# Optimization experiments

Hardware: AMD Instinct MI355X
Metric: run time of the kernel (lower is better)

The kernel has to match this reference:

```python
import jax, jax.numpy as jnp
import numpy as np

NUM_LEVELS = 4
RADIUS = 4


def setup_inputs() -> dict:
    key = jax.random.key(0)
    k1, k2, k3 = jax.random.split(key, 3)
    B, C, H, W = 2, 256, 64, 64
    N = 4
    fmap1 = jax.random.normal(k1, (B, C, H, W), dtype=jnp.float32)
    fmap2 = jax.random.normal(k2, (B, C, H, W), dtype=jnp.float32)
    # coords channel 0 = x in [0, W-1], channel 1 = y in [0, H-1]
    coords = jax.random.uniform(k3, (B, N, 2, H, W), dtype=jnp.float32) * (W - 1)
    return {"fmap1": fmap1, "fmap2": fmap2, "coords": coords}


def _bilinear_gather(corr, x, y):
    """Zero-padded bilinear sampling (grid_sample align_corners=True semantics).
    corr: (B, P, h2, w2) per-query-pixel correlation maps.
    x, y: (B, N, P, K2) absolute pixel coords into (w2, h2).
    Returns (B, N, P, K2)."""
    Bv, P, h2, w2 = corr.shape
    x0 = jnp.floor(x)
    y0 = jnp.floor(y)
    wx1 = x - x0
    wy1 = y - y0
    b = jnp.arange(Bv)[:, None, None, None]
    p = jnp.arange(P)[None, None, :, None]

    def corner(yi, xi):
        valid = (xi >= 0) & (xi <= w2 - 1) & (yi >= 0) & (yi <= h2 - 1)
        xi_c = jnp.clip(xi, 0, w2 - 1).astype(jnp.int32)
        yi_c = jnp.clip(yi, 0, h2 - 1).astype(jnp.int32)
        v = corr[b, p, yi_c, xi_c]
        return jnp.where(valid, v, jnp.zeros((), corr.dtype))

    v00 = corner(y0, x0)
    v01 = corner(y0, x0 + 1)
    v10 = corner(y0 + 1, x0)
    v11 = corner(y0 + 1, x0 + 1)
    return ((1 - wy1) * (1 - wx1) * v00 + (1 - wy1) * wx1 * v01
            + wy1 * (1 - wx1) * v10 + wy1 * wx1 * v11)


def reference(fmap1, fmap2, coords):
    B, C, H, W = fmap1.shape
    _, N = coords.shape[0], coords.shape[1]
    P = H * W
    r = RADIUS
    K = 2 * r + 1
    K2 = K * K

    # All-pairs correlation: (B, P_query, H2, W2), scaled by 1/sqrt(C) (RAFT)
    f1 = fmap1.reshape(B, C, P)
    f2 = fmap2.reshape(B, C, P)
    corr = jnp.einsum('bcp,bcq->bpq', f1, f2) / jnp.sqrt(jnp.asarray(C, fmap1.dtype))
    corr = corr.reshape(B, P, H, W)

    # Pyramid via 2x2 average pooling (stride 2, no padding)
    pyramid = [corr]
    c = corr
    for _ in range(NUM_LEVELS - 1):
        h2, w2 = c.shape[-2:]
        c = c.reshape(B, P, h2 // 2, 2, w2 // 2, 2).mean(axis=(3, 5))
        pyramid.append(c)

    # Window offsets. Faithful to the torch code: delta = stack(meshgrid(dy, dx, 'ij'))
    # so delta[...,0] = yy is added to the x-channel, delta[...,1] = xx to the y-channel.
    d = jnp.linspace(-r, r, K).astype(coords.dtype)
    yy, xx = jnp.meshgrid(d, d, indexing='ij')
    off_x = yy.reshape(1, 1, 1, K2)  # added to coords[...,0]
    off_y = xx.reshape(1, 1, 1, K2)  # added to coords[...,1]

    cx = coords[:, :, 0].reshape(B, N, P)  # (B, N, P)
    cy = coords[:, :, 1].reshape(B, N, P)

    outs = []
    for i, cl in enumerate(pyramid):
        scale = jnp.asarray(2.0 ** i, coords.dtype)
        x = cx[..., None] / scale + off_x  # (B, N, P, K2)
        y = cy[..., None] / scale + off_y
        v = _bilinear_gather(cl, x, y)     # (B, N, P, K2)
        outs.append(v.reshape(B, N, H, W, K2))

    out = jnp.concatenate(outs, axis=-1)   # (B, N, H, W, L*K2)
    Ctot = out.shape[-1]
    # Matches torch: contiguous (B,N,H,W,C) reshaped row-major to (B, N*C, H, W)
    out = out.reshape(B, N * Ctot, H, W)
    return out.astype(jnp.float32)
```

## Files before the change

### kernel.cpp

```cpp
#include <hip/hip_runtime.h>
#include <hip/hip_bf16.h>
#include <cstdint>

#define B_    2
#define C_    256
#define H_    64
#define W_    64
#define P_    (H_*W_)
#define N_    4
#define RAD   4
#define K2_   81
#define CTOT  (4*K2_)

typedef __bf16 bf16x8 __attribute__((ext_vector_type(8)));
typedef float  f32x4  __attribute__((ext_vector_type(4)));

__device__ __forceinline__ void gload_lds16(const void* g, void* l) {
    __builtin_amdgcn_global_load_lds(
        (const __attribute__((address_space(1))) void*)g,
        (__attribute__((address_space(3))) void*)l,
        16, 0, 0);
}

__global__ void transpose_cvt(const float* __restrict__ in0,
                              const float* __restrict__ in1,
                              __hip_bfloat16* __restrict__ out0,
                              __hip_bfloat16* __restrict__ out1) {
    __shared__ float tile[32][33];
    const int z     = blockIdx.z;
    const int which = z >> 1;
    const int b     = z & 1;
    const float* in          = which ? in1  : in0;
    __hip_bfloat16* out      = which ? out1 : out0;
    const int p0 = blockIdx.x * 32;
    const int c0 = blockIdx.y * 32;
    const int tx = threadIdx.x;
    const int ty = threadIdx.y;
    const float* src = in + ((size_t)b * C_ + c0) * P_ + p0;
    #pragma unroll
    for (int i = 0; i < 32; i += 8)
        tile[ty + i][tx] = src[(size_t)(ty + i) * P_ + tx];
    __syncthreads();
    __hip_bfloat16* dst = out + ((size_t)b * P_ + p0) * C_ + c0;
    #pragma unroll
    for (int i = 0; i < 32; i += 8)
        dst[(size_t)(ty + i) * C_ + tx] = __float2bfloat16(tile[tx][ty + i]);
}

#define TSTR 136

__global__ __launch_bounds__(256) void gemm_corr(
    const short* __restrict__ f1t,
    const short* __restrict__ f2t,
    __hip_bfloat16* __restrict__ corr0,
    __hip_bfloat16* __restrict__ corr1)
{
    __shared__ short smem[128 * TSTR];
    short* As = smem;
    short* Bs = smem + 8192;

    const int tid  = threadIdx.x;
    const int lane = tid & 63;
    const int wv   = tid >> 6;
    const int wm   = (wv >> 1) * 64;
    const int wn   = (wv & 1) * 64;
    const int b    = blockIdx.z;
    const int bx   = blockIdx.x;
    const int m0   = blockIdx.y * 128;
    const int n0   = bx * 128;
    const int qd   = lane >> 4;
    const int l15  = lane & 15;

    const short* gA[4];
    const short* gB[4];
    int ldsOff[4];
    #pragma unroll
    for (int it = 0; it < 4; ++it) {
        const int ci = it * 256 + tid;
        const int r  = ci >> 3;
        const int cp = ci & 7;
        const int kc = cp ^ (r & 7);
        gA[it] = f1t + ((size_t)(b * P_ + m0 + r)) * C_ + kc * 8;
        gB[it] = f2t + ((size_t)(b * P_ + n0 + r)) * C_ + kc * 8;
        ldsOff[it] = (it * 256 + wv * 64) * 8;
    }

    int aAddr[4][2], bAddr[4][2];
    #pragma unroll
    for (int i = 0; i < 4; ++i) {
        const int m = wm + i * 16 + l15;
        const int n = wn + i * 16 + l15;
        #pragma unroll
        for (int s = 0; s < 2; ++s) {
            const int lc = s * 4 + qd;
            aAddr[i][s] = m * 64 + ((lc ^ (m & 7)) * 8);
            bAddr[i][s] = n * 64 + ((lc ^ (n & 7)) * 8);
        }
    }

    f32x4 zero = {0.f, 0.f, 0.f, 0.f};
    f32x4 acc[4][4];
    #pragma unroll
    for (int mi = 0; mi < 4; ++mi)
        #pragma unroll
        for (int ni = 0; ni < 4; ++ni)
            acc[mi][ni] = zero;

    for (int kt = 0; kt < 4; ++kt) {
        const int k0 = kt * 64;
        #pragma unroll
        for (int it = 0; it < 4; ++it) {
            gload_lds16(gA[it] + k0, As + ldsOff[it]);
            gload_lds16(gB[it] + k0, Bs + ldsOff[it]);
        }
        __syncthreads();
        #pragma unroll
        for (int s = 0; s < 2; ++s) {
            bf16x8 af[4], bfr[4];
            #pragma unroll
            for (int i = 0; i < 4; ++i) {
                af[i]  = *(const bf16x8*)(As + aAddr[i][s]);
                bfr[i] = *(const bf16x8*)(Bs + bAddr[i][s]);
            }
            #pragma unroll
            for (int mi = 0; mi < 4; ++mi)
                #pragma unroll
                for (int ni = 0; ni < 4; ++ni)
                    acc[mi][ni] = __builtin_amdgcn_mfma_f32_16x16x32_bf16(
                        af[mi], bfr[ni], acc[mi][ni], 0, 0, 0);
        }
        __syncthreads();
    }

    const float sc = 0.0625f;
    __hip_bfloat16* tile = (__hip_bfloat16*)smem;
    #pragma unroll
    for (int mi = 0; mi < 4; ++mi) {
        #pragma unroll
        for (int ni = 0; ni < 4; ++ni) {
            #pragma unroll
            for (int r = 0; r < 4; ++r) {
                const int rl = wm + mi * 16 + qd * 4 + r;
                const int cl = wn + ni * 16 + l15;
                tile[rl * TSTR + cl] = __float2bfloat16(acc[mi][ni][r] * sc);
            }
        }
    }
    __syncthreads();

    #pragma unroll
    for (int i = 0; i < 8; ++i) {
        const int cid = i * 256 + tid;
        const int tr  = cid >> 4;
        const int tc  = cid & 15;
        const float4 v = *(const float4*)(smem + tr * TSTR + tc * 8);
        *(float4*)(corr0 + ((size_t)(b * P_ + m0 + tr)) * P_ + n0 + tc * 8) = v;
    }

    #pragma unroll
    for (int i = 0; i < 16; ++i) {
        const int oid = i * 256 + tid;
        const int pr  = oid >> 5;
        const int pc  = oid & 31;
        const uint32_t u0 = *(const uint32_t*)(smem + pr * TSTR + 2 * pc);
        const uint32_t u1 = *(const uint32_t*)(smem + pr * TSTR + 64 + 2 * pc);
        const float a0 = __uint_as_float(u0 << 16);
        const float a1 = __uint_as_float(u0 & 0xffff0000u);
        const float b0 = __uint_as_float(u1 << 16);
        const float b1 = __uint_as_float(u1 & 0xffff0000u);
        corr1[((size_t)(b * P_ + m0 + pr)) * 1024 + bx * 32 + pc] =
            __float2bfloat16((a0 + a1 + b0 + b1) * 0.25f);
    }
}

#define SEL4(e, a0, a1, a2, a3) ((e)==0?(a0):(e)==1?(a1):(e)==2?(a2):(a3))

__global__ __launch_bounds__(256) void gather3(
    const float* __restrict__ coords,
    const __hip_bfloat16* __restrict__ c0,
    const __hip_bfloat16* __restrict__ c1,
    float* __restrict__ out) {
    __shared__ float pool_sm[320];
    __shared__ float patch[4][440];
    const int tid  = threadIdx.x;
    const int lane = tid & 63;
    const int n    = tid >> 6;
    const int bp   = blockIdx.x;
    const int b    = bp >> 12;
    const int p    = bp & (P_ - 1);

    const __hip_bfloat16* c0b = c0 + (size_t)bp * 4096;
    const __hip_bfloat16* c1b = c1 + (size_t)bp * 1024;

    {
        const int y2 = tid >> 4, x2 = tid & 15;
        const uint32_t u0 = *(const uint32_t*)(c1b + (2 * y2) * 32 + 2 * x2);
        const uint32_t u1 = *(const uint32_t*)(c1b + (2 * y2 + 1) * 32 + 2 * x2);
        const float a0 = __uint_as_float(u0 << 16);
        const float a1 = __uint_as_float(u0 & 0xffff0000u);
        const float b0 = __uint_as_float(u1 << 16);
        const float b1 = __uint_as_float(u1 & 0xffff0000u);
        pool_sm[tid] = (a0 + a1 + b0 + b1) * 0.25f;
    }
    __syncthreads();
    if (tid < 64) {
        const int y3 = tid >> 3, x3 = tid & 7;
        const float* r0 = pool_sm + (2 * y3) * 16 + 2 * x3;
        pool_sm[256 + tid] = (r0[0] + r0[1] + r0[16] + r0[17]) * 0.25f;
    }
    __syncthreads();

    const float cx = coords[((size_t)((b * N_ + n) * 2 + 0)) * P_ + p];
    const float cy = coords[((size_t)((b * N_ + n) * 2 + 1)) * P_ + p];

    int x0i[4], y0i[4];
    float w00[4], w01[4], w10[4], w11[4];
    #pragma unroll
    for (int l = 0; l < 4; ++l) {
        const float inv = 1.0f / (float)(1 << l);
        const float x = cx * inv, y = cy * inv;
        const float x0f = floorf(x), y0f = floorf(y);
        const float wx = x - x0f, wy = y - y0f;
        x0i[l] = (int)x0f - RAD;
        y0i[l] = (int)y0f - RAD;
        w00[l] = (1.f - wy) * (1.f - wx);
        w01[l] = (1.f - wy) * wx;
        w10[l] = wy * (1.f - wx);
        w11[l] = wy * wx;
    }

    float* pw = patch[n];

    #pragma unroll
    for (int it = 0; it < 7; ++it) {
        const int idx = it * 64 + lane;
        if (idx < 440) {
            const int lvl = idx / 110;
            const int rem = idx - lvl * 110;
            const int r   = rem / 11;
            const int cc  = rem - r * 11;
            if (cc < 10) {
                const int hw = H_ >> lvl;
                const int gr = SEL4(lvl, y0i[0], y0i[1], y0i[2], y0i[3]) + r;
                const int gc = SEL4(lvl, x0i[0], x0i[1], x0i[2], x0i[3]) + cc;
                const bool ok = (gr >= 0) & (gr < hw) & (gc >= 0) & (gc < hw);
                float v = 0.f;
                if (ok) {
                    if (lvl < 2) {
                        const __hip_bfloat16* cp = (lvl == 0) ? c0b : c1b;
                        v = __bfloat162float(cp[gr * hw + gc]);
                    } else {
                        const int li = (lvl == 2) ? (gr * 16 + gc)
                                                  : (256 + gr * 8 + gc);
                        v = pool_sm[li];
                    }
                }
                pw[idx] = v;
            }
        }
    }

    const size_t obase = ((size_t)(b * N_ + n) * P_ + p) * CTOT;
    #pragma unroll
    for (int it = 0; it < 6; ++it) {
        const int o = it * 64 + lane;
        if (o < CTOT) {
            const int lvl = o / K2_;
            const int k2  = o - lvl * K2_;
            const int ki  = k2 / 9;
            const int kj  = k2 - ki * 9;
            const float* pr = pw + lvl * 110 + kj * 11 + ki;
            const float a = SEL4(lvl, w00[0], w00[1], w00[2], w00[3]);
            const float bq = SEL4(lvl, w01[0], w01[1], w01[2], w01[3]);
            const float c = SEL4(lvl, w10[0], w10[1], w10[2], w10[3]);
            const float d = SEL4(lvl, w11[0], w11[1], w11[2], w11[3]);
            out[obase + o] = a * pr[0] + bq * pr[1] + c * pr[11] + d * pr[12];
        }
    }
}

extern "C" void kernel_launch(void* const* d_in, const int* in_sizes, int n_in,
                              void* d_out, int out_size, void* d_ws, size_t ws_size,
                              hipStream_t stream) {
    const float* fmap1  = (const float*)d_in[0];
    const float* fmap2  = (const float*)d_in[1];
    const float* coords = (const float*)d_in[2];
    float* out = (float*)d_out;

    char* ws = (char*)d_ws;
    __hip_bfloat16* f1t = (__hip_bfloat16*)ws;
    __hip_bfloat16* f2t = (__hip_bfloat16*)(ws + 4194304);
    __hip_bfloat16* c0  = (__hip_bfloat16*)(ws + 8388608);
    __hip_bfloat16* c1  = (__hip_bfloat16*)(ws + 75497472);

    {
        dim3 grid(P_ / 32, C_ / 32, 2 * B_);
        dim3 blk(32, 8);
        transpose_cvt<<<grid, blk, 0, stream>>>(fmap1, fmap2, f1t, f2t);
    }

    {
        dim3 grid(P_ / 128, P_ / 128, B_);
        gemm_corr<<<grid, 256, 0, stream>>>((const short*)f1t, (const short*)f2t,
                                            c0, c1);
    }

    gather3<<<B_ * P_, 256, 0, stream>>>(coords, c0, c1, out);
}
```

Baseline: 127.0 us.

## Double-buffer GEMM K tiles and restructure gather per-level patch loads

The correlation GEMM now keeps two LDS buffers and prefetches the next K tile with direct global-to-LDS loads while MFMAs run on the current one, replacing the load-sync-compute-sync loop. LDS use per block grows to 64 KB, which may lower occupancy. The gather kernel computes per-level integer bases and bilinear weights in four lanes and shares them through LDS, so the per-element SEL4 select chains and per-thread weight registers go away. Its patch fill is split into explicit per-level loops with unsigned bounds checks.

Measured after the change: 129.9 us. 1.02x slower.

```diff
diff --git a/kernel.cpp b/kernel.cpp
--- a/kernel.cpp
+++ b/kernel.cpp
@@ -55,9 +55,7 @@
     __hip_bfloat16* __restrict__ corr0,
     __hip_bfloat16* __restrict__ corr1)
 {
-    __shared__ short smem[128 * TSTR];
-    short* As = smem;
-    short* Bs = smem + 8192;
+    __shared__ short smem[32768];
 
     const int tid  = threadIdx.x;
     const int lane = tid & 63;
@@ -106,14 +104,26 @@
         for (int ni = 0; ni < 4; ++ni)
             acc[mi][ni] = zero;
 
+    #pragma unroll
+    for (int it = 0; it < 4; ++it) {
+        gload_lds16(gA[it], smem + ldsOff[it]);
+        gload_lds16(gB[it], smem + 8192 + ldsOff[it]);
+    }
+
+    #pragma unroll
     for (int kt = 0; kt < 4; ++kt) {
-        const int k0 = kt * 64;
-        #pragma unroll
-        for (int it = 0; it < 4; ++it) {
-            gload_lds16(gA[it] + k0, As + ldsOff[it]);
-            gload_lds16(gB[it] + k0, Bs + ldsOff[it]);
-        }
         __syncthreads();
+        if (kt < 3) {
+            const int nxt = ((kt + 1) & 1) * 16384;
+            const int k0  = (kt + 1) * 64;
+            #pragma unroll
+            for (int it = 0; it < 4; ++it) {
+                gload_lds16(gA[it] + k0, smem + nxt + ldsOff[it]);
+                gload_lds16(gB[it] + k0, smem + nxt + 8192 + ldsOff[it]);
+            }
+        }
+        const short* As = smem + (kt & 1) * 16384;
+        const short* Bs = As + 8192;
         #pragma unroll
         for (int s = 0; s < 2; ++s) {
             bf16x8 af[4], bfr[4];
@@ -129,8 +139,8 @@
                     acc[mi][ni] = __builtin_amdgcn_mfma_f32_16x16x32_bf16(
                         af[mi], bfr[ni], acc[mi][ni], 0, 0, 0);
         }
-        __syncthreads();
-    }
+    }
+    __syncthreads();
 
     const float sc = 0.0625f;
     __hip_bfloat16* tile = (__hip_bfloat16*)smem;
@@ -173,15 +183,16 @@
     }
 }
 
-#define SEL4(e, a0, a1, a2, a3) ((e)==0?(a0):(e)==1?(a1):(e)==2?(a2):(a3))
-
-__global__ __launch_bounds__(256) void gather3(
+__global__ __launch_bounds__(256) void gather4(
     const float* __restrict__ coords,
     const __hip_bfloat16* __restrict__ c0,
     const __hip_bfloat16* __restrict__ c1,
     float* __restrict__ out) {
     __shared__ float pool_sm[320];
     __shared__ float patch[4][440];
+    __shared__ int   gsm[4][8];
+    __shared__ float wsm[4][4][4];
+
     const int tid  = threadIdx.x;
     const int lane = tid & 63;
     const int n    = tid >> 6;
@@ -212,50 +223,63 @@
 
     const float cx = coords[((size_t)((b * N_ + n) * 2 + 0)) * P_ + p];
     const float cy = coords[((size_t)((b * N_ + n) * 2 + 1)) * P_ + p];
-
-    int x0i[4], y0i[4];
-    float w00[4], w01[4], w10[4], w11[4];
-    #pragma unroll
-    for (int l = 0; l < 4; ++l) {
-        const float inv = 1.0f / (float)(1 << l);
+    if (lane < 4) {
+        const int l = lane;
+        const float inv = (l == 0) ? 1.f : (l == 1) ? 0.5f : (l == 2) ? 0.25f : 0.125f;
         const float x = cx * inv, y = cy * inv;
         const float x0f = floorf(x), y0f = floorf(y);
         const float wx = x - x0f, wy = y - y0f;
-        x0i[l] = (int)x0f - RAD;
-        y0i[l] = (int)y0f - RAD;
-        w00[l] = (1.f - wy) * (1.f - wx);
-        w01[l] = (1.f - wy) * wx;
-        w10[l] = wy * (1.f - wx);
-        w11[l] = wy * wx;
+        gsm[n][l]     = (int)x0f - RAD;
+        gsm[n][4 + l] = (int)y0f - RAD;
+        wsm[n][l][0] = (1.f - wy) * (1.f - wx);
+        wsm[n][l][1] = (1.f - wy) * wx;
+        wsm[n][l][2] = wy * (1.f - wx);
+        wsm[n][l][3] = wy * wx;
     }
 
     float* pw = patch[n];
 
     #pragma unroll
-    for (int it = 0; it < 7; ++it) {
-        const int idx = it * 64 + lane;
-        if (idx < 440) {
-            const int lvl = idx / 110;
-            const int rem = idx - lvl * 110;
-            const int r   = rem / 11;
-            const int cc  = rem - r * 11;
-            if (cc < 10) {
-                const int hw = H_ >> lvl;
-                const int gr = SEL4(lvl, y0i[0], y0i[1], y0i[2], y0i[3]) + r;
-                const int gc = SEL4(lvl, x0i[0], x0i[1], x0i[2], x0i[3]) + cc;
-                const bool ok = (gr >= 0) & (gr < hw) & (gc >= 0) & (gc < hw);
+    for (int lvl = 0; lvl < 2; ++lvl) {
+        const __hip_bfloat16* src = lvl ? c1b : c0b;
+        const int hw = lvl ? 32 : 64;
+        const int sh = lvl ? 5 : 6;
+        const int xb = gsm[n][lvl];
+        const int yb = gsm[n][4 + lvl];
+        #pragma unroll
+        for (int it = 0; it < 2; ++it) {
+            const int idx = it * 64 + lane;
+            if (idx < 110) {
+                const int r  = idx / 11;
+                const int cc = idx - r * 11;
+                const int gr = yb + r, gc = xb + cc;
                 float v = 0.f;
-                if (ok) {
-                    if (lvl < 2) {
-                        const __hip_bfloat16* cp = (lvl == 0) ? c0b : c1b;
-                        v = __bfloat162float(cp[gr * hw + gc]);
-                    } else {
-                        const int li = (lvl == 2) ? (gr * 16 + gc)
-                                                  : (256 + gr * 8 + gc);
-                        v = pool_sm[li];
-                    }
-                }
-                pw[idx] = v;
+                if ((cc < 10) & ((unsigned)gr < (unsigned)hw) &
+                    ((unsigned)gc < (unsigned)hw))
+                    v = __bfloat162float(src[(gr << sh) + gc]);
+                pw[lvl * 110 + idx] = v;
+            }
+        }
+    }
+    #pragma unroll
+    for (int lvl = 2; lvl < 4; ++lvl) {
+        const int hw   = (lvl == 2) ? 16 : 8;
+        const int sh   = (lvl == 2) ? 4 : 3;
+        const int base = (lvl == 2) ? 0 : 256;
+        const int xb = gsm[n][lvl];
+        const int yb = gsm[n][4 + lvl];
+        #pragma unroll
+        for (int it = 0; it < 2; ++it) {
+            const int idx = it * 64 + lane;
+            if (idx < 110) {
+                const int r  = idx / 11;
+                const int cc = idx - r * 11;
+                const int gr = yb + r, gc = xb + cc;
+                float v = 0.f;
+                if ((cc < 10) & ((unsigned)gr < (unsigned)hw) &
+                    ((unsigned)gc < (unsigned)hw))
+                    v = pool_sm[base + (gr << sh) + gc];
+                pw[lvl * 110 + idx] = v;
             }
         }
     }
@@ -269,12 +293,10 @@
             const int k2  = o - lvl * K2_;
             const int ki  = k2 / 9;
             const int kj  = k2 - ki * 9;
+            const float4 w = *(const float4*)&wsm[n][lvl][0];
             const float* pr = pw + lvl * 110 + kj * 11 + ki;
-            const float a = SEL4(lvl, w00[0], w00[1], w00[2], w00[3]);
-            const float bq = SEL4(lvl, w01[0], w01[1], w01[2], w01[3]);
-            const float c = SEL4(lvl, w10[0], w10[1], w10[2], w10[3]);
-            const float d = SEL4(lvl, w11[0], w11[1], w11[2], w11[3]);
-            out[obase + o] = a * pr[0] + bq * pr[1] + c * pr[11] + d * pr[12];
+            out[obase + o] = w.x * pr[0] + w.y * pr[1] +
+                             w.z * pr[11] + w.w * pr[12];
         }
     }
 }
@@ -305,5 +327,5 @@
                                             c0, c1);
     }
 
-    gather3<<<B_ * P_, 256, 0, stream>>>(coords, c0, c1, out);
-}
+    gather4<<<B_ * P_, 256, 0, stream>>>(coords, c0, c1, out);
+}
```
